# Optimization experiments

Hardware: AMD Instinct MI355X
Metric: run time of the kernel (lower is better)

## Reference

```python
import jax, jax.numpy as jnp
import numpy as np

B, N, DIN, DOUT = 8, 2048, 256, 256
ALPHA = 0.2  # leaky relu slope
EPS = 1e-6


def setup_inputs() -> dict:
    key = jax.random.key(0)
    k1, k2, k3, k4 = jax.random.split(key, 4)
    h = jax.random.normal(k1, (B, N, DIN), dtype=jnp.float32)
    adj = jax.random.uniform(k2, (B, N, N), dtype=jnp.float32)
    # xavier_uniform with gain=1.414
    gain = 1.414
    limW = gain * np.sqrt(6.0 / (DIN + DOUT))
    W = jax.random.uniform(k3, (DIN, DOUT), minval=-limW, maxval=limW, dtype=jnp.float32)
    lima = gain * np.sqrt(6.0 / (2 * DOUT + 1))
    a = jax.random.uniform(k4, (2 * DOUT, 1), minval=-lima, maxval=lima, dtype=jnp.float32)
    return {"h": h, "adj": adj, "W": W, "a": a}


def reference(h, adj, W, a):
    # Wh: [B, N, DOUT]
    Wh = jnp.einsum("bnd,df->bnf", h, W)
    # Split additive attention: cat([Wh_i, Wh_j]) @ a == Wh_i @ a1 + Wh_j @ a2
    a1 = a[:DOUT, 0]   # [DOUT]
    a2 = a[DOUT:, 0]   # [DOUT]
    s1 = Wh @ a1       # [B, N] score contribution of source node i
    s2 = Wh @ a2       # [B, N] score contribution of target node j
    e = s1[:, :, None] + s2[:, None, :]           # [B, N, N]
    e = jnp.where(e > 0, e, ALPHA * e)            # leaky relu
    e = e + jnp.log(adj + EPS)                    # soft adjacency mask
    alpha_w = jax.nn.softmax(e, axis=-1)          # [B, N, N]
    # dropout is identity in eval / deterministic reference
    h_prime = jnp.einsum("bij,bjf->bif", alpha_w, Wh)
    return h_prime
```

## Files before the change

kernel.cpp:

```cpp
#include <hip/hip_runtime.h>
#include <hip/hip_bf16.h>
#include <stdint.h>

#define ALPHA_ 0.2f
#define EPS_   1e-6f

typedef __attribute__((ext_vector_type(8))) short  short8;
typedef __attribute__((ext_vector_type(4))) float  float4v;

static __device__ __forceinline__ unsigned short f2bf(float x) {
    union { float f; unsigned int u; } c; c.f = x;
    return (unsigned short)((c.u + 0x7fffu + ((c.u >> 16) & 1u)) >> 16);
}

__global__ __launch_bounds__(256) void k_wt(const float* __restrict__ W,
                                            unsigned short* __restrict__ WTs) {
    const int g  = blockIdx.x * 256 + threadIdx.x;
    const int fb = g >> 9, kc = (g >> 6) & 7, l = g & 63;
    const int m = l & 15, quad = l >> 4;
    const int f = fb * 16 + m, d0 = kc * 32 + quad * 8;
    unsigned short v[8];
#pragma unroll
    for (int i = 0; i < 8; ++i) v[i] = f2bf(W[(d0 + i) * 256 + f]);
    uint4 o;
    o.x = (unsigned)v[0] | ((unsigned)v[1] << 16);
    o.y = (unsigned)v[2] | ((unsigned)v[3] << 16);
    o.z = (unsigned)v[4] | ((unsigned)v[5] << 16);
    o.w = (unsigned)v[6] | ((unsigned)v[7] << 16);
    *(uint4*)(WTs + (size_t)g * 8) = o;
}

__global__ __launch_bounds__(512) void k_wh(const float* __restrict__ h,
                                            const unsigned short* __restrict__ WTs,
                                            const float* __restrict__ a,
                                            unsigned short* __restrict__ WhS,
                                            float* __restrict__ s1g,
                                            float* __restrict__ s2g) {
    __shared__ __align__(16) unsigned short A_lds[32][264];
    __shared__ __align__(16) unsigned short T_lds[256][40];
    __shared__ float s1p[32], s2p[32];
    const int t    = threadIdx.x;
    const int lane = t & 63;
    const int wv   = t >> 6;
    const int m    = lane & 15;
    const int quad = lane >> 4;
    const int r0   = blockIdx.x * 32;
    const int b    = blockIdx.x >> 6;
    const int jc   = blockIdx.x & 63;
    const int j0   = r0 & 2047;

    if (t < 32) { s1p[t] = 0.f; s2p[t] = 0.f; }

#pragma unroll
    for (int k = 0; k < 4; ++k) {
        const int flat = t + k * 512;
        const int r  = flat >> 6;
        const int d4 = flat & 63;
        float4v hv = *(const float4v*)(h + (size_t)(r0 + r) * 256 + d4 * 4);
        uint2 pk;
        pk.x = (unsigned)f2bf(hv.x) | ((unsigned)f2bf(hv.y) << 16);
        pk.y = (unsigned)f2bf(hv.z) | ((unsigned)f2bf(hv.w) << 16);
        *(uint2*)&A_lds[r][d4 * 4] = pk;
    }
    __syncthreads();

    const int fbase = wv * 32;
    float4v acc[2][2];
#pragma unroll
    for (int it = 0; it < 2; ++it)
#pragma unroll
        for (int ft = 0; ft < 2; ++ft)
#pragma unroll
            for (int r = 0; r < 4; ++r) acc[it][ft][r] = 0.f;

    const unsigned short* wtb = WTs + (size_t)(wv * 2) * 4096 + lane * 8;

#pragma unroll
    for (int kc = 0; kc < 8; ++kc) {
        short8 af0 = *(const short8*)&A_lds[m][kc * 32 + quad * 8];
        short8 af1 = *(const short8*)&A_lds[16 + m][kc * 32 + quad * 8];
#pragma unroll
        for (int ft = 0; ft < 2; ++ft) {
            short8 bf = *(const short8*)(wtb + (size_t)ft * 4096 + kc * 512);
            acc[0][ft] = __builtin_amdgcn_mfma_f32_16x16x32_bf16(af0, bf, acc[0][ft], 0, 0, 0);
            acc[1][ft] = __builtin_amdgcn_mfma_f32_16x16x32_bf16(af1, bf, acc[1][ft], 0, 0, 0);
        }
    }

    float a1v[2], a2v[2];
#pragma unroll
    for (int ft = 0; ft < 2; ++ft) {
        a1v[ft] = a[fbase + ft * 16 + m];
        a2v[ft] = a[256 + fbase + ft * 16 + m];
    }
#pragma unroll
    for (int it = 0; it < 2; ++it) {
#pragma unroll
        for (int reg = 0; reg < 4; ++reg) {
            float v1 = 0.f, v2 = 0.f;
#pragma unroll
            for (int ft = 0; ft < 2; ++ft) {
                const float c = acc[it][ft][reg];
                v1 = fmaf(c, a1v[ft], v1);
                v2 = fmaf(c, a2v[ft], v2);
            }
            v1 += __shfl_xor(v1, 1); v2 += __shfl_xor(v2, 1);
            v1 += __shfl_xor(v1, 2); v2 += __shfl_xor(v2, 2);
            v1 += __shfl_xor(v1, 4); v2 += __shfl_xor(v2, 4);
            v1 += __shfl_xor(v1, 8); v2 += __shfl_xor(v2, 8);
            if (m == 0) {
                const int row = it * 16 + quad * 4 + reg;
                atomicAdd(&s1p[row], v1);
                atomicAdd(&s2p[row], v2);
            }
        }
    }

#pragma unroll
    for (int it = 0; it < 2; ++it)
#pragma unroll
        for (int ft = 0; ft < 2; ++ft)
#pragma unroll
            for (int reg = 0; reg < 4; ++reg)
                T_lds[fbase + ft * 16 + m][it * 16 + quad * 4 + reg] =
                    f2bf(acc[it][ft][reg]);

    __syncthreads();

#pragma unroll
    for (int e = 0; e < 2; ++e) {
        const int idx = e * 512 + t;
        const int fb = idx >> 6, l = idx & 63;
        uint4 v = *(const uint4*)&T_lds[fb * 16 + (l & 15)][(l >> 4) * 8];
        *(uint4*)(WhS + ((size_t)(b * 64 + jc) * 16 + fb) * 512 + l * 8) = v;
    }

    if (t < 32) {
        s1g[(size_t)b * 2048 + j0 + t] = s1p[t];
        s2g[(size_t)b * 2048 + j0 + t] = s2p[t];
    }
}

static __device__ __forceinline__ unsigned pk2bf(float lo, float hi) {
    float2 v; v.x = lo; v.y = hi;
    union { __hip_bfloat162 h2; unsigned u; } cv;
    cv.h2 = __float22bfloat162_rn(v);
    return cv.u;
}

static __device__ __forceinline__ uint2 pquad(float4v av, float4v s2v,
                                              float s1, float& rs) {
    float e0 = s1 + s2v.x, e1 = s1 + s2v.y, e2 = s1 + s2v.z, e3 = s1 + s2v.w;
    e0 = fmaxf(e0, ALPHA_ * e0); e1 = fmaxf(e1, ALPHA_ * e1);
    e2 = fmaxf(e2, ALPHA_ * e2); e3 = fmaxf(e3, ALPHA_ * e3);
    const float p0 = (av.x + EPS_) * __expf(e0);
    const float p1 = (av.y + EPS_) * __expf(e1);
    const float p2 = (av.z + EPS_) * __expf(e2);
    const float p3 = (av.w + EPS_) * __expf(e3);
    rs += (p0 + p1) + (p2 + p3);
    uint2 r;
    r.x = pk2bf(p0, p1);
    r.y = pk2bf(p2, p3);
    return r;
}

__global__ __launch_bounds__(512, 4) void k_attn(const float* __restrict__ adj,
                                                 const unsigned short* __restrict__ WhS,
                                                 const float* __restrict__ s1g,
                                                 const float* __restrict__ s2g,
                                                 float* __restrict__ out) {
    __shared__ __align__(16) unsigned short pbuf[2][32][140];
    __shared__ float rsum_lds[32];

    const int t    = threadIdx.x;
    const int lane = t & 63;
    const int wv   = t >> 6;
    const int m    = lane & 15;
    const int quad = lane >> 4;
    const int blk  = blockIdx.x;
    const int b    = blk & 7;
    const int i0   = (blk >> 3) * 32;

    const int ip = t >> 4;
    const int jq = t & 15;

    const float* adjp = adj + (size_t)(b * 2048 + i0 + ip) * 2048 + jq * 8;
    const float* s2p  = s2g + (size_t)b * 2048 + jq * 8;
    const float  s1v  = s1g[(size_t)b * 2048 + i0 + ip];

    const int fbb = wv * 2;
    const unsigned short* whs = WhS + (size_t)b * 64 * 16 * 512;

    float4v acc[2][2];
#pragma unroll
    for (int it = 0; it < 2; ++it)
#pragma unroll
        for (int ft = 0; ft < 2; ++ft)
#pragma unroll
            for (int r = 0; r < 4; ++r) acc[it][ft][r] = 0.f;

    float rs = 0.f;

    float4v adjv[2], s2v[2];
#pragma unroll
    for (int c = 0; c < 2; ++c) {
        adjv[c] = *(const float4v*)(adjp + c * 4);
        s2v[c]  = *(const float4v*)(s2p + c * 4);
    }

    for (int step = 0; step < 16; ++step) {
        const int cur = step & 1;

#pragma unroll
        for (int c = 0; c < 2; ++c) {
            uint2 pk = pquad(adjv[c], s2v[c], s1v, rs);
            *(uint2*)&pbuf[cur][ip][jq * 8 + c * 4] = pk;
        }

        const int ns = (step + 1) & 15;
#pragma unroll
        for (int c = 0; c < 2; ++c) {
            adjv[c] = *(const float4v*)(adjp + (size_t)ns * 128 + c * 4);
            s2v[c]  = *(const float4v*)(s2p + (size_t)ns * 128 + c * 4);
        }

        __syncthreads();

#pragma unroll
        for (int kc = 0; kc < 4; ++kc) {
            const unsigned short* bp =
                whs + ((size_t)((step * 4 + kc) * 16 + fbb)) * 512 + lane * 8;
            short8 bf0 = *(const short8*)bp;
            short8 bf1 = *(const short8*)(bp + 512);
            short8 af0 = *(const short8*)&pbuf[cur][m][kc * 32 + quad * 8];
            short8 af1 = *(const short8*)&pbuf[cur][16 + m][kc * 32 + quad * 8];
            acc[0][0] = __builtin_amdgcn_mfma_f32_16x16x32_bf16(af0, bf0, acc[0][0], 0, 0, 0);
            acc[0][1] = __builtin_amdgcn_mfma_f32_16x16x32_bf16(af0, bf1, acc[0][1], 0, 0, 0);
            acc[1][0] = __builtin_amdgcn_mfma_f32_16x16x32_bf16(af1, bf0, acc[1][0], 0, 0, 0);
            acc[1][1] = __builtin_amdgcn_mfma_f32_16x16x32_bf16(af1, bf1, acc[1][1], 0, 0, 0);
        }
    }

    rs += __shfl_xor(rs, 1);
    rs += __shfl_xor(rs, 2);
    rs += __shfl_xor(rs, 4);
    rs += __shfl_xor(rs, 8);
    if (jq == 0) rsum_lds[ip] = rs;
    __syncthreads();

#pragma unroll
    for (int reg = 0; reg < 4; ++reg) {
        const int row  = quad * 4 + reg;
        const float i0v = 1.0f / rsum_lds[row];
        const float i1v = 1.0f / rsum_lds[16 + row];
#pragma unroll
        for (int ft = 0; ft < 2; ++ft) {
            const int f = wv * 32 + ft * 16 + m;
            out[(size_t)(b * 2048 + i0 + row) * 256 + f]      = acc[0][ft][reg] * i0v;
            out[(size_t)(b * 2048 + i0 + 16 + row) * 256 + f] = acc[1][ft][reg] * i1v;
        }
    }
}

extern "C" void kernel_launch(void* const* d_in, const int* in_sizes, int n_in,
                              void* d_out, int out_size, void* d_ws, size_t ws_size,
                              hipStream_t stream) {
    const float* h   = (const float*)d_in[0];
    const float* adj = (const float*)d_in[1];
    const float* W   = (const float*)d_in[2];
    const float* a   = (const float*)d_in[3];
    float* out = (float*)d_out;

    unsigned short* WhS = (unsigned short*)d_ws;
    unsigned short* WTs = (unsigned short*)((char*)d_ws + 8388608);
    float*          s1  = (float*)((char*)d_ws + 8388608 + 131072);
    float*          s2  = s1 + 16384;

    k_wt  <<<dim3(32),   dim3(256), 0, stream>>>(W, WTs);
    k_wh  <<<dim3(512),  dim3(512), 0, stream>>>(h, WTs, a, WhS, s1, s2);
    k_attn<<<dim3(512),  dim3(512), 0, stream>>>(adj, WhS, s1, s2, out);
}
```

Measured before the change: 235.5 us.

## Software-pipeline attention loop with 64-wide steps, register-prefetched B and LDS s2

Restructures the attention main loop into 32 steps of 64 columns. Probability computation for the next tile now overlaps with the MFMAs of the current tile, using one barrier per step instead of separate produce and consume phases. The Wh B-fragments are prefetched into registers one step ahead, and s2 is staged once in LDS instead of being reloaded from global memory each step. This trades a small LDS footprint change and higher register pressure (double-buffered B registers at 4 waves/SIMD bound) for better latency hiding.

```diff
diff --git a/kernel.cpp b/kernel.cpp
--- a/kernel.cpp
+++ b/kernel.cpp
@@ -169,7 +169,8 @@
                                                  const float* __restrict__ s1g,
                                                  const float* __restrict__ s2g,
                                                  float* __restrict__ out) {
-    __shared__ __align__(16) unsigned short pbuf[2][32][140];
+    __shared__ __align__(16) unsigned short pbuf[2][32][72];
+    __shared__ __align__(16) float s2_lds[2048];
     __shared__ float rsum_lds[32];
 
     const int t    = threadIdx.x;
@@ -184,12 +185,16 @@
     const int ip = t >> 4;
     const int jq = t & 15;
 
-    const float* adjp = adj + (size_t)(b * 2048 + i0 + ip) * 2048 + jq * 8;
-    const float* s2p  = s2g + (size_t)b * 2048 + jq * 8;
+    const float* adjp = adj + (size_t)(b * 2048 + i0 + ip) * 2048 + jq * 4;
     const float  s1v  = s1g[(size_t)b * 2048 + i0 + ip];
 
     const int fbb = wv * 2;
-    const unsigned short* whs = WhS + (size_t)b * 64 * 16 * 512;
+    const unsigned short* whs = WhS + (size_t)b * 64 * 16 * 512 + lane * 8;
+
+    {
+        const float* s2src = s2g + (size_t)b * 2048;
+        *(float4v*)&s2_lds[t * 4] = *(const float4v*)(s2src + t * 4);
+    }
 
     float4v acc[2][2];
 #pragma unroll
@@ -201,45 +206,79 @@
 
     float rs = 0.f;
 
-    float4v adjv[2], s2v[2];
-#pragma unroll
-    for (int c = 0; c < 2; ++c) {
-        adjv[c] = *(const float4v*)(adjp + c * 4);
-        s2v[c]  = *(const float4v*)(s2p + c * 4);
-    }
-
-    for (int step = 0; step < 16; ++step) {
-        const int cur = step & 1;
-
-#pragma unroll
-        for (int c = 0; c < 2; ++c) {
-            uint2 pk = pquad(adjv[c], s2v[c], s1v, rs);
-            *(uint2*)&pbuf[cur][ip][jq * 8 + c * 4] = pk;
-        }
-
-        const int ns = (step + 1) & 15;
-#pragma unroll
-        for (int c = 0; c < 2; ++c) {
-            adjv[c] = *(const float4v*)(adjp + (size_t)ns * 128 + c * 4);
-            s2v[c]  = *(const float4v*)(s2p + (size_t)ns * 128 + c * 4);
-        }
-
+    short8  bregA[4], bregB[4];
+    float4v adjA, adjB;
+
+    adjA = *(const float4v*)(adjp);
+    adjB = *(const float4v*)(adjp + 64);
+    {
+        const unsigned short* bp = whs;
+        bregA[0] = *(const short8*)(bp + (size_t)(fbb) * 512);
+        bregA[1] = *(const short8*)(bp + (size_t)(fbb + 1) * 512);
+        bregA[2] = *(const short8*)(bp + (size_t)(16 + fbb) * 512);
+        bregA[3] = *(const short8*)(bp + (size_t)(17 + fbb) * 512);
+    }
+    __syncthreads();
+    {
+        float4v s2v = *(const float4v*)&s2_lds[jq * 4];
+        uint2 pk = pquad(adjA, s2v, s1v, rs);
+        *(uint2*)&pbuf[0][ip][jq * 4] = pk;
+    }
+    __syncthreads();
+
+#define PHASE_LOADS(sB, breg_, adj_, sA)                                        \
+    {                                                                           \
+        const unsigned short* bp = whs + (size_t)((sB) * 32 + fbb) * 512;       \
+        breg_[0] = *(const short8*)bp;                                          \
+        breg_[1] = *(const short8*)(bp + 512);                                  \
+        breg_[2] = *(const short8*)(bp + 16 * 512);                             \
+        breg_[3] = *(const short8*)(bp + 17 * 512);                             \
+        adj_ = *(const float4v*)(adjp + (size_t)(sA) * 64);                     \
+    }
+
+#define PHASE_MFMA(buf, breg_)                                                  \
+    _Pragma("unroll")                                                           \
+    for (int kc = 0; kc < 2; ++kc) {                                            \
+        short8 af0 = *(const short8*)&pbuf[buf][m][kc * 32 + quad * 8];         \
+        short8 af1 = *(const short8*)&pbuf[buf][16 + m][kc * 32 + quad * 8];    \
+        acc[0][0] = __builtin_amdgcn_mfma_f32_16x16x32_bf16(af0, breg_[kc*2],   acc[0][0], 0, 0, 0); \
+        acc[0][1] = __builtin_amdgcn_mfma_f32_16x16x32_bf16(af0, breg_[kc*2+1], acc[0][1], 0, 0, 0); \
+        acc[1][0] = __builtin_amdgcn_mfma_f32_16x16x32_bf16(af1, breg_[kc*2],   acc[1][0], 0, 0, 0); \
+        acc[1][1] = __builtin_amdgcn_mfma_f32_16x16x32_bf16(af1, breg_[kc*2+1], acc[1][1], 0, 0, 0); \
+    }
+
+#define PHASE_P(sp, adj_, buf)                                                  \
+    {                                                                           \
+        float4v s2v = *(const float4v*)&s2_lds[(sp) * 64 + jq * 4];             \
+        uint2 pk = pquad(adj_, s2v, s1v, rs);                                   \
+        *(uint2*)&pbuf[buf][ip][jq * 4] = pk;                                   \
+    }
+
+    for (int s = 0; s < 30; s += 2) {
+        PHASE_LOADS(s + 1, bregB, adjA, s + 2)
+        PHASE_MFMA(0, bregA)
+        PHASE_P(s + 1, adjB, 1)
         __syncthreads();
-
-#pragma unroll
-        for (int kc = 0; kc < 4; ++kc) {
-            const unsigned short* bp =
-                whs + ((size_t)((step * 4 + kc) * 16 + fbb)) * 512 + lane * 8;
-            short8 bf0 = *(const short8*)bp;
-            short8 bf1 = *(const short8*)(bp + 512);
-            short8 af0 = *(const short8*)&pbuf[cur][m][kc * 32 + quad * 8];
-            short8 af1 = *(const short8*)&pbuf[cur][16 + m][kc * 32 + quad * 8];
-            acc[0][0] = __builtin_amdgcn_mfma_f32_16x16x32_bf16(af0, bf0, acc[0][0], 0, 0, 0);
-            acc[0][1] = __builtin_amdgcn_mfma_f32_16x16x32_bf16(af0, bf1, acc[0][1], 0, 0, 0);
-            acc[1][0] = __builtin_amdgcn_mfma_f32_16x16x32_bf16(af1, bf0, acc[1][0], 0, 0, 0);
-            acc[1][1] = __builtin_amdgcn_mfma_f32_16x16x32_bf16(af1, bf1, acc[1][1], 0, 0, 0);
-        }
-    }
+        PHASE_LOADS(s + 2, bregA, adjB, s + 3)
+        PHASE_MFMA(1, bregB)
+        PHASE_P(s + 2, adjA, 0)
+        __syncthreads();
+    }
+    {
+        const unsigned short* bp = whs + (size_t)(31 * 32 + fbb) * 512;
+        bregB[0] = *(const short8*)bp;
+        bregB[1] = *(const short8*)(bp + 512);
+        bregB[2] = *(const short8*)(bp + 16 * 512);
+        bregB[3] = *(const short8*)(bp + 17 * 512);
+    }
+    PHASE_MFMA(0, bregA)
+    PHASE_P(31, adjB, 1)
+    __syncthreads();
+    PHASE_MFMA(1, bregB)
+
+#undef PHASE_LOADS
+#undef PHASE_MFMA
+#undef PHASE_P
 
     rs += __shfl_xor(rs, 1);
     rs += __shfl_xor(rs, 2);
```

Result: slower. 251.9 us (+7.0%).
